# Kernel tuning notes

Measured on AMD Instinct MI355X. Metric: run time of the kernel, lower is better.

Reference implementation:

```python
import jax, jax.numpy as jnp
import numpy as np

NUM_HEADS = 8
EPS = 1e-12  # torch F.normalize default eps


def setup_inputs() -> dict:
    key = jax.random.key(0)
    k0, k1, k2, k3 = jax.random.split(key, 4)
    b, c, d, h, w = 2, 64, 8, 128, 128
    x = jax.random.normal(k0, (b, c, d, h, w), dtype=jnp.float32)
    # 1x1x1 conv weights stored as [out, in]; depthwise 3x3x3 as [out, 1, kd, kh, kw]
    w_qkv = jax.random.normal(k1, (3 * c, c), dtype=jnp.float32) * 0.05
    w_dw = jax.random.normal(k2, (3 * c, 1, 3, 3, 3), dtype=jnp.float32) * 0.05
    temperature = jnp.ones((NUM_HEADS, 1, 1), dtype=jnp.float32)
    w_proj = jax.random.normal(k3, (c, c), dtype=jnp.float32) * 0.05
    return {"x": x, "w_qkv": w_qkv, "w_dw": w_dw, "temperature": temperature, "w_proj": w_proj}


def _l2norm(t):
    # F.normalize(t, dim=-1): t / max(||t||, eps)
    n = jnp.sqrt(jnp.sum(t * t, axis=-1, keepdims=True))
    return t / jnp.maximum(n, EPS)


def reference(x, w_qkv, w_dw, temperature, w_proj):
    b, c, d, h, w = x.shape
    heads = NUM_HEADS
    ch = c // heads  # per-head channel dim
    # 1x1x1 conv (pointwise) -> einsum over channels
    qkv = jnp.einsum('bcdhw,oc->bodhw', x, w_qkv)
    # depthwise 3x3x3 conv, padding 1 (SAME), groups = 3*c
    qkv = jax.lax.conv_general_dilated(
        qkv, w_dw, window_strides=(1, 1, 1), padding=[(1, 1)] * 3,
        feature_group_count=3 * c,
        dimension_numbers=('NCDHW', 'OIDHW', 'NCDHW'))
    q, k, v = jnp.split(qkv, 3, axis=1)
    n = d * h * w
    q = q.reshape(b, heads, ch, n)
    k = k.reshape(b, heads, ch, n)
    v = v.reshape(b, heads, ch, n)
    q = _l2norm(q)
    k = _l2norm(k)
    # channel-channel attention: [b, heads, ch, ch]
    attn = jnp.einsum('bhcn,bhen->bhce', q, k) * temperature
    attn = jax.nn.softmax(attn, axis=-1)
    out = jnp.einsum('bhce,bhen->bhcn', attn, v)
    out = out.reshape(b, c, d, h, w)
    out = jnp.einsum('bcdhw,oc->bodhw', out, w_proj)
    return out
```

## Files before the change

kernel.cpp:

```cpp
#include <hip/hip_runtime.h>
#include <math.h>

#define NPOS 131072
#define GC 128

typedef __attribute__((ext_vector_type(8))) short short8v;
typedef __attribute__((ext_vector_type(4))) float f32x4;
typedef __attribute__((address_space(3))) unsigned int lds_u32;
typedef const __attribute__((address_space(1))) unsigned int glb_u32;

__device__ __forceinline__ void bf16split(float x, unsigned short& hi, unsigned short& lo) {
  unsigned u = __float_as_uint(x);
  hi = (unsigned short)(u >> 16);
  float hif = __uint_as_float(u & 0xffff0000u);
  float l = x - hif;
  lo = (unsigned short)(__float_as_uint(l) >> 16);
}

__global__ void k_prep(const float* __restrict__ w_qkv, unsigned short* __restrict__ whi,
                       unsigned short* __restrict__ wlo) {
  int idx = blockIdx.x * 256 + threadIdx.x;
  if (idx < 12288) {
    int j = idx & 7, l = (idx >> 3) & 63, ks = (idx >> 9) & 1, ot = (idx >> 10) & 3,
        g = idx >> 12;
    int out = ot * 16 + (l & 15);
    int k = ks * 32 + (l >> 4) * 8 + j;
    bf16split(w_qkv[(g * 64 + out) * 64 + k], whi[idx], wlo[idx]);
  }
}

__device__ __forceinline__ void stage_async(const float* __restrict__ gb, float* lbuf,
                                            int tid) {
#pragma unroll
  for (int r = 0; r < 4; ++r) {
    int idx = r * 256 + tid;
    int ch = idx >> 4, f4 = idx & 15;
    __builtin_amdgcn_global_load_lds((glb_u32*)(gb + (size_t)ch * NPOS + f4 * 4),
                                     (lds_u32*)(lbuf + idx * 4), 16, 0, 0);
  }
}

__device__ __forceinline__ void pw_compute(const float (*xl)[64], const short8v* ahi,
                                           const short8v* alo, float* __restrict__ ob0,
                                           int lane) {
  const int prow = lane & 15, kgrp = lane >> 4;
#pragma unroll
  for (int pt = 0; pt < 4; ++pt) {
    const int pos = pt * 16 + prow;
    short8v bh[2], bl[2];
#pragma unroll
    for (int ks = 0; ks < 2; ++ks)
#pragma unroll
      for (int j = 0; j < 8; ++j) {
        unsigned short h, lo16;
        bf16split(xl[ks * 32 + kgrp * 8 + j][pos], h, lo16);
        bh[ks][j] = (short)h;
        bl[ks][j] = (short)lo16;
      }
    f32x4 D = {0.f, 0.f, 0.f, 0.f};
#pragma unroll
    for (int ks = 0; ks < 2; ++ks) {
      D = __builtin_amdgcn_mfma_f32_16x16x32_bf16(ahi[ks], bh[ks], D, 0, 0, 0);
      D = __builtin_amdgcn_mfma_f32_16x16x32_bf16(ahi[ks], bl[ks], D, 0, 0, 0);
      D = __builtin_amdgcn_mfma_f32_16x16x32_bf16(alo[ks], bh[ks], D, 0, 0, 0);
    }
    float* ob = ob0 + pos;
#pragma unroll
    for (int jj = 0; jj < 4; ++jj) ob[(size_t)jj * NPOS] = D[jj];
  }
}

__global__ __launch_bounds__(256) void k_pw_mfma(const float* __restrict__ x,
                                                 const unsigned short* __restrict__ whi,
                                                 const unsigned short* __restrict__ wlo,
                                                 float* __restrict__ pre) {
  const int b = blockIdx.y;
  const int lane = threadIdx.x & 63;
  const int ot = threadIdx.x >> 6;
  const int p0 = blockIdx.x * 256;
  __shared__ __align__(16) float xl[2][64][64];
  short8v ahi[2], alo[2];
#pragma unroll
  for (int ks = 0; ks < 2; ++ks) {
    int fi = ((ot * 2 + ks) * 64 + lane) * 8;
    ahi[ks] = *(const short8v*)&whi[fi];
    alo[ks] = *(const short8v*)&wlo[fi];
  }
  const float* xb = x + ((size_t)b * 64) * NPOS + p0;
  const int tid = threadIdx.x;
  float* ob0 = pre + ((size_t)b * 64 + ot * 16 + (lane >> 4) * 4) * NPOS + p0;
  stage_async(xb, &xl[0][0][0], tid);
  __syncthreads();
#pragma unroll
  for (int t = 0; t < 4; ++t) {
    if (t < 3) stage_async(xb + (t + 1) * 64, &xl[(t + 1) & 1][0][0], tid);
    pw_compute(xl[t & 1], ahi, alo, ob0 + t * 64, lane);
    __syncthreads();
  }
}

__device__ __forceinline__ void stage_tile(float (*t)[10][40], const float* __restrict__ in,
                                           int h0, int w0, int tid) {
  for (int i = tid; i < 800; i += 256) {
    int j = i & 7, row = i >> 3;
    int h = row % 10, dpl = row / 10;
    int dd = dpl - 1, hh = h0 + h - 1;
    float4 v = make_float4(0.f, 0.f, 0.f, 0.f);
    if (dd >= 0 && dd < 8 && hh >= 0 && hh < 128)
      v = *(const float4*)&in[((size_t)dd * 128 + hh) * 128 + (w0 + j * 4)];
    *(float4*)&t[dpl][h][4 + j * 4] = v;
  }
  for (int i = tid; i < 200; i += 256) {
    int side = i & 1, row = i >> 1;
    int h = row % 10, dpl = row / 10;
    int dd = dpl - 1, hh = h0 + h - 1;
    int ww = side ? (w0 + 32) : (w0 - 1);
    float v = 0.f;
    if (dd >= 0 && dd < 8 && hh >= 0 && hh < 128 && ww >= 0 && ww < 128)
      v = in[((size_t)dd * 128 + hh) * 128 + ww];
    t[dpl][h][side ? 36 : 3] = v;
  }
}

__device__ __forceinline__ void conv_droll(const float (*t)[10][40], const float* wk,
                                           int hl, int wl, float* acc) {
#pragma unroll
  for (int d = 0; d < 8; ++d) acc[d] = 0.f;
#pragma unroll
  for (int dpl = 0; dpl < 10; ++dpl) {
#pragma unroll
    for (int kh = 0; kh < 3; ++kh) {
#pragma unroll
      for (int kw = 0; kw < 3; ++kw) {
        float f = t[dpl][hl + kh][3 + wl + kw];
#pragma unroll
        for (int kd = 0; kd < 3; ++kd) {
          const int d = dpl - kd;
          if (d >= 0 && d < 8)
            acc[d] = fmaf(f, wk[(kd * 3 + kh) * 3 + kw], acc[d]);
        }
      }
    }
  }
}

__global__ __launch_bounds__(256) void k_dw(const float* __restrict__ pre,
                                            const float* __restrict__ w_dw,
                                            float* __restrict__ conv,
                                            float* __restrict__ nsq, int g) {
  const int id = blockIdx.x;
  const int sid = (id & 7) * 1024 + (id >> 3);
  const int z = sid >> 6, r = sid & 63, by = r >> 2, bx = r & 3;
  const int b = z >> 6;
  const int c = z & 63;
  const int h0 = by * 8;
  const int w0 = bx * 32;
  __shared__ float t[10][10][40];
  __shared__ float red[4];
  const int tid = threadIdx.y * 32 + threadIdx.x;
  stage_tile(t, pre + ((size_t)b * 64 + c) * NPOS, h0, w0, tid);
  float wk[27];
#pragma unroll
  for (int i = 0; i < 27; ++i) wk[i] = w_dw[(g * 64 + c) * 27 + i];
  __syncthreads();
  const int wl = threadIdx.x, hl = threadIdx.y;
  float acc[8];
  conv_droll(t, wk, hl, wl, acc);
  float* outp = conv + ((size_t)b * 64 + c) * NPOS + (size_t)(h0 + hl) * 128 + (w0 + wl);
  float nsum = 0.f;
#pragma unroll
  for (int d = 0; d < 8; ++d) {
    outp[(size_t)d * 16384] = acc[d];
    nsum = fmaf(acc[d], acc[d], nsum);
  }
  if (nsq) {
    const int lane = tid & 63, wv = tid >> 6;
    float v = nsum;
    v += __shfl_down(v, 32); v += __shfl_down(v, 16); v += __shfl_down(v, 8);
    v += __shfl_down(v, 4);  v += __shfl_down(v, 2);  v += __shfl_down(v, 1);
    if (lane == 0) red[wv] = v;
    __syncthreads();
    if (tid == 0) {
      const int blk = by * 4 + bx;
      nsq[((size_t)b * 64 + c) * 64 + blk] = red[0] + red[1] + red[2] + red[3];
    }
  }
}

__global__ __launch_bounds__(256) void k_gramS(const float* __restrict__ qconv,
                                               const float* __restrict__ kconv,
                                               float* __restrict__ partialS) {
  const int chunk = blockIdx.x;
  const int bh = blockIdx.y;
  const int b = bh >> 3, head = bh & 7;
  const int tid = threadIdx.x;
  const size_t base = ((size_t)b * 64 + head * 8) * NPOS + (size_t)chunk * 1024 + tid;
  const float* qb = qconv + base;
  const float* kb = kconv + base;
  float S[64];
#pragma unroll
  for (int i = 0; i < 64; ++i) S[i] = 0.f;
#pragma unroll
  for (int it = 0; it < 4; ++it) {
    const size_t off = (size_t)it * 256;
    float qv[8], kv[8];
#pragma unroll
    for (int c = 0; c < 8; ++c) qv[c] = qb[(size_t)c * NPOS + off];
#pragma unroll
    for (int e = 0; e < 8; ++e) kv[e] = kb[(size_t)e * NPOS + off];
#pragma unroll
    for (int c = 0; c < 8; ++c)
#pragma unroll
      for (int e = 0; e < 8; ++e) S[c * 8 + e] = fmaf(qv[c], kv[e], S[c * 8 + e]);
  }
#pragma unroll
  for (int i = 0; i < 64; ++i) asm volatile("" : "+v"(S[i]));

  const int lane = tid & 63, wv = tid >> 6;
#define BSTEP(src, dst, n, s)                                        \
  {                                                                  \
    const bool hi_ = (lane >> (s)) & 1;                              \
    _Pragma("unroll")                                                \
    for (int i_ = 0; i_ < (n); ++i_) {                               \
      float send_ = hi_ ? src[i_] : src[i_ + (n)];                   \
      float mine_ = hi_ ? src[i_ + (n)] : src[i_];                   \
      dst[i_] = mine_ + __shfl_xor(send_, 1 << (s));                 \
    }                                                                \
  }
  float v32[32], v16[16], v8[8], v4[4], v2[2], v1[1];
  BSTEP(S,   v32, 32, 0)
  BSTEP(v32, v16, 16, 1)
  BSTEP(v16, v8,   8, 2)
  BSTEP(v8,  v4,   4, 3)
  BSTEP(v4,  v2,   2, 4)
  BSTEP(v2,  v1,   1, 5)
#undef BSTEP
  const int idx = ((lane & 1) << 5) | ((lane & 2) << 3) | ((lane & 4) << 1) |
                  ((lane & 8) >> 1) | ((lane & 16) >> 3) | ((lane & 32) >> 5);
  __shared__ float red[4][64];
  red[wv][idx] = v1[0];
  __syncthreads();
  if (tid < 64) {
    float s = red[0][tid] + red[1][tid] + red[2][tid] + red[3][tid];
    partialS[((size_t)bh * GC + chunk) * 64 + tid] = s;
  }
}

__global__ void k_attn(const float* __restrict__ partialS, const float* __restrict__ nqp,
                       const float* __restrict__ nkp, const float* __restrict__ temp,
                       float* __restrict__ A) {
  const int bh = blockIdx.x;
  const int b = bh >> 3, head = bh & 7;
  const int tid = threadIdx.x;
  __shared__ float sums[80];
  if (tid < 64) {
    float s = 0.f;
    const float* pp = partialS + (size_t)bh * GC * 64 + tid;
    for (int j = 0; j < GC; ++j) s += pp[j * 64];
    sums[tid] = s;
  } else if (tid < 72) {
    const int e = tid - 64;
    float s = 0.f;
    const float* pp = nkp + ((size_t)b * 64 + head * 8 + e) * 64;
    for (int j = 0; j < 64; ++j) s += pp[j];
    sums[64 + e] = s;
  } else if (tid < 80) {
    const int c = tid - 72;
    float s = 0.f;
    const float* pp = nqp + ((size_t)b * 64 + head * 8 + c) * 64;
    for (int j = 0; j < 64; ++j) s += pp[j];
    sums[72 + c] = s;
  }
  __syncthreads();
  if (tid < 8) {
    const int c = tid;
    float tp = temp[head];
    float qd = fmaxf(sqrtf(sums[72 + c]), 1e-12f);
    float vals[8];
    float mx = -1e30f;
#pragma unroll
    for (int e = 0; e < 8; ++e) {
      float kd = fmaxf(sqrtf(sums[64 + e]), 1e-12f);
      vals[e] = sums[c * 8 + e] / (qd * kd) * tp;
      mx = fmaxf(mx, vals[e]);
    }
    float den = 0.f;
#pragma unroll
    for (int e = 0; e < 8; ++e) { vals[e] = expf(vals[e] - mx); den += vals[e]; }
#pragma unroll
    for (int e = 0; e < 8; ++e) A[bh * 64 + c * 8 + e] = vals[e] / den;
  }
}

__global__ void k_M(const float* __restrict__ w_proj, const float* __restrict__ A,
                    unsigned short* __restrict__ Mhi, unsigned short* __restrict__ Mlo) {
  const int b = blockIdx.x;
  for (int e = threadIdx.x; e < 4096; e += 256) {
    int j = e & 7, l = (e >> 3) & 63, ks = (e >> 9) & 1, ot = (e >> 10) & 3;
    int out = ot * 16 + (l & 15);
    int gch = ks * 32 + (l >> 4) * 8 + j;
    int hg = gch >> 3, jj = gch & 7;
    float s = 0.f;
#pragma unroll
    for (int i = 0; i < 8; ++i)
      s += w_proj[out * 64 + hg * 8 + i] * A[(b * 8 + hg) * 64 + i * 8 + jj];
    bf16split(s, Mhi[b * 4096 + e], Mlo[b * 4096 + e]);
  }
}

__global__ __launch_bounds__(256) void k_out_mfma(const float* __restrict__ vconv,
                                                  const unsigned short* __restrict__ Mhi,
                                                  const unsigned short* __restrict__ Mlo,
                                                  float* __restrict__ out) {
  const int b = blockIdx.y;
  const int lane = threadIdx.x & 63;
  const int ot = threadIdx.x >> 6;
  const int p0 = blockIdx.x * 256;
  __shared__ __align__(16) float xl[2][64][64];
  short8v ahi[2], alo[2];
#pragma unroll
  for (int ks = 0; ks < 2; ++ks) {
    int fi = b * 4096 + ((ot * 2 + ks) * 64 + lane) * 8;
    ahi[ks] = *(const short8v*)&Mhi[fi];
    alo[ks] = *(const short8v*)&Mlo[fi];
  }
  const float* vb = vconv + ((size_t)b * 64) * NPOS + p0;
  const int tid = threadIdx.x;
  float* ob0 = out + ((size_t)b * 64 + ot * 16 + (lane >> 4) * 4) * NPOS + p0;
  stage_async(vb, &xl[0][0][0], tid);
  __syncthreads();
#pragma unroll
  for (int t = 0; t < 4; ++t) {
    if (t < 3) stage_async(vb + (t + 1) * 64, &xl[(t + 1) & 1][0][0], tid);
    pw_compute(xl[t & 1], ahi, alo, ob0 + t * 64, lane);
    __syncthreads();
  }
}

extern "C" void kernel_launch(void* const* d_in, const int* in_sizes, int n_in,
                              void* d_out, int out_size, void* d_ws, size_t ws_size,
                              hipStream_t stream) {
  const float* x      = (const float*)d_in[0];
  const float* w_qkv  = (const float*)d_in[1];
  const float* w_dw   = (const float*)d_in[2];
  const float* temp   = (const float*)d_in[3];
  const float* w_proj = (const float*)d_in[4];
  float* out = (float*)d_out;
  float* ws  = (float*)d_ws;

  float* conv_buf = ws;
  float* kconv    = conv_buf + 16777216ull;
  float* nqp      = kconv + 16777216ull;
  float* nkp      = nqp + 8192ull;
  float* partialS = nkp + 8192ull;
  float* Abuf     = partialS + 131072ull;
  unsigned short* whi = (unsigned short*)(Abuf + 1024ull);
  unsigned short* wlo = whi + 12288ull;
  unsigned short* Mhi = wlo + 12288ull;
  unsigned short* Mlo = Mhi + 8192ull;

  k_prep<<<48, 256, 0, stream>>>(w_qkv, whi, wlo);
  k_pw_mfma<<<dim3(512, 2), 256, 0, stream>>>(x, whi, wlo, out);
  k_dw<<<8192, dim3(32, 8), 0, stream>>>(out, w_dw, conv_buf, nqp, 0);
  k_pw_mfma<<<dim3(512, 2), 256, 0, stream>>>(x, whi + 4096, wlo + 4096, out);
  k_dw<<<8192, dim3(32, 8), 0, stream>>>(out, w_dw, kconv, nkp, 1);
  k_gramS<<<dim3(GC, 16), 256, 0, stream>>>(conv_buf, kconv, partialS);
  k_attn<<<16, 128, 0, stream>>>(partialS, nqp, nkp, temp, Abuf);
  k_M<<<2, 256, 0, stream>>>(w_proj, Abuf, Mhi, Mlo);
  k_pw_mfma<<<dim3(512, 2), 256, 0, stream>>>(x, whi + 8192, wlo + 8192, out);
  k_dw<<<8192, dim3(32, 8), 0, stream>>>(out, w_dw, conv_buf, nullptr, 2);
  k_out_mfma<<<dim3(512, 2), 256, 0, stream>>>(conv_buf, Mhi, Mlo, out);
}
```

Baseline: 231.9 us.

## Stage pointwise MFMA outputs through LDS for coalesced stores, one tile per block

```diff
diff --git a/kernel.cpp b/kernel.cpp
--- a/kernel.cpp
+++ b/kernel.cpp
@@ -6,8 +6,6 @@
 
 typedef __attribute__((ext_vector_type(8))) short short8v;
 typedef __attribute__((ext_vector_type(4))) float f32x4;
-typedef __attribute__((address_space(3))) unsigned int lds_u32;
-typedef const __attribute__((address_space(1))) unsigned int glb_u32;
 
 __device__ __forceinline__ void bf16split(float x, unsigned short& hi, unsigned short& lo) {
   unsigned u = __float_as_uint(x);
@@ -29,21 +27,22 @@
   }
 }
 
-__device__ __forceinline__ void stage_async(const float* __restrict__ gb, float* lbuf,
-                                            int tid) {
+__device__ __forceinline__ void pw_body(const float* __restrict__ gin,
+                                        const short8v* ahi, const short8v* alo,
+                                        float* __restrict__ gout, int tid) {
+  __shared__ __align__(16) float xl[64][66];
+  const int lane = tid & 63;
+  const int ot = tid >> 6;
+  const int f4 = tid & 15;
 #pragma unroll
   for (int r = 0; r < 4; ++r) {
-    int idx = r * 256 + tid;
-    int ch = idx >> 4, f4 = idx & 15;
-    __builtin_amdgcn_global_load_lds((glb_u32*)(gb + (size_t)ch * NPOS + f4 * 4),
-                                     (lds_u32*)(lbuf + idx * 4), 16, 0, 0);
-  }
-}
-
-__device__ __forceinline__ void pw_compute(const float (*xl)[64], const short8v* ahi,
-                                           const short8v* alo, float* __restrict__ ob0,
-                                           int lane) {
+    int ch2 = (r * 256 + tid) >> 4;
+    float4 g = *(const float4*)&gin[(size_t)ch2 * NPOS + f4 * 4];
+    *(float4*)&xl[ch2][f4 * 4] = g;
+  }
+  __syncthreads();
   const int prow = lane & 15, kgrp = lane >> 4;
+  f32x4 Dv[4];
 #pragma unroll
   for (int pt = 0; pt < 4; ++pt) {
     const int pos = pt * 16 + prow;
@@ -64,9 +63,20 @@
       D = __builtin_amdgcn_mfma_f32_16x16x32_bf16(ahi[ks], bl[ks], D, 0, 0, 0);
       D = __builtin_amdgcn_mfma_f32_16x16x32_bf16(alo[ks], bh[ks], D, 0, 0, 0);
     }
-    float* ob = ob0 + pos;
-#pragma unroll
-    for (int jj = 0; jj < 4; ++jj) ob[(size_t)jj * NPOS] = D[jj];
+    Dv[pt] = D;
+  }
+  __syncthreads();
+#pragma unroll
+  for (int pt = 0; pt < 4; ++pt)
+#pragma unroll
+    for (int jj = 0; jj < 4; ++jj)
+      xl[ot * 16 + kgrp * 4 + jj][pt * 16 + prow] = Dv[pt][jj];
+  __syncthreads();
+#pragma unroll
+  for (int r = 0; r < 4; ++r) {
+    int idx = r * 256 + tid;
+    int row = idx >> 4;
+    *(float4*)&gout[(size_t)row * NPOS + f4 * 4] = *(const float4*)&xl[row][f4 * 4];
   }
 }
 
@@ -77,8 +87,7 @@
   const int b = blockIdx.y;
   const int lane = threadIdx.x & 63;
   const int ot = threadIdx.x >> 6;
-  const int p0 = blockIdx.x * 256;
-  __shared__ __align__(16) float xl[2][64][64];
+  const int p0 = blockIdx.x * 64;
   short8v ahi[2], alo[2];
 #pragma unroll
   for (int ks = 0; ks < 2; ++ks) {
@@ -86,17 +95,8 @@
     ahi[ks] = *(const short8v*)&whi[fi];
     alo[ks] = *(const short8v*)&wlo[fi];
   }
-  const float* xb = x + ((size_t)b * 64) * NPOS + p0;
-  const int tid = threadIdx.x;
-  float* ob0 = pre + ((size_t)b * 64 + ot * 16 + (lane >> 4) * 4) * NPOS + p0;
-  stage_async(xb, &xl[0][0][0], tid);
-  __syncthreads();
-#pragma unroll
-  for (int t = 0; t < 4; ++t) {
-    if (t < 3) stage_async(xb + (t + 1) * 64, &xl[(t + 1) & 1][0][0], tid);
-    pw_compute(xl[t & 1], ahi, alo, ob0 + t * 64, lane);
-    __syncthreads();
-  }
+  pw_body(x + ((size_t)b * 64) * NPOS + p0, ahi, alo,
+          pre + ((size_t)b * 64) * NPOS + p0, threadIdx.x);
 }
 
 __device__ __forceinline__ void stage_tile(float (*t)[10][40], const float* __restrict__ in,
@@ -315,8 +315,7 @@
   const int b = blockIdx.y;
   const int lane = threadIdx.x & 63;
   const int ot = threadIdx.x >> 6;
-  const int p0 = blockIdx.x * 256;
-  __shared__ __align__(16) float xl[2][64][64];
+  const int p0 = blockIdx.x * 64;
   short8v ahi[2], alo[2];
 #pragma unroll
   for (int ks = 0; ks < 2; ++ks) {
@@ -324,17 +323,8 @@
     ahi[ks] = *(const short8v*)&Mhi[fi];
     alo[ks] = *(const short8v*)&Mlo[fi];
   }
-  const float* vb = vconv + ((size_t)b * 64) * NPOS + p0;
-  const int tid = threadIdx.x;
-  float* ob0 = out + ((size_t)b * 64 + ot * 16 + (lane >> 4) * 4) * NPOS + p0;
-  stage_async(vb, &xl[0][0][0], tid);
-  __syncthreads();
-#pragma unroll
-  for (int t = 0; t < 4; ++t) {
-    if (t < 3) stage_async(vb + (t + 1) * 64, &xl[(t + 1) & 1][0][0], tid);
-    pw_compute(xl[t & 1], ahi, alo, ob0 + t * 64, lane);
-    __syncthreads();
-  }
+  pw_body(vconv + ((size_t)b * 64) * NPOS + p0, ahi, alo,
+          out + ((size_t)b * 64) * NPOS + p0, threadIdx.x);
 }
 
 extern "C" void kernel_launch(void* const* d_in, const int* in_sizes, int n_in,
@@ -360,14 +350,14 @@
   unsigned short* Mlo = Mhi + 8192ull;
 
   k_prep<<<48, 256, 0, stream>>>(w_qkv, whi, wlo);
-  k_pw_mfma<<<dim3(512, 2), 256, 0, stream>>>(x, whi, wlo, out);
+  k_pw_mfma<<<dim3(2048, 2), 256, 0, stream>>>(x, whi, wlo, out);
   k_dw<<<8192, dim3(32, 8), 0, stream>>>(out, w_dw, conv_buf, nqp, 0);
-  k_pw_mfma<<<dim3(512, 2), 256, 0, stream>>>(x, whi + 4096, wlo + 4096, out);
+  k_pw_mfma<<<dim3(2048, 2), 256, 0, stream>>>(x, whi + 4096, wlo + 4096, out);
   k_dw<<<8192, dim3(32, 8), 0, stream>>>(out, w_dw, kconv, nkp, 1);
   k_gramS<<<dim3(GC, 16), 256, 0, stream>>>(conv_buf, kconv, partialS);
   k_attn<<<16, 128, 0, stream>>>(partialS, nqp, nkp, temp, Abuf);
   k_M<<<2, 256, 0, stream>>>(w_proj, Abuf, Mhi, Mlo);
-  k_pw_mfma<<<dim3(512, 2), 256, 0, stream>>>(x, whi + 8192, wlo + 8192, out);
+  k_pw_mfma<<<dim3(2048, 2), 256, 0, stream>>>(x, whi + 8192, wlo + 8192, out);
   k_dw<<<8192, dim3(32, 8), 0, stream>>>(out, w_dw, conv_buf, nullptr, 2);
-  k_out_mfma<<<dim3(512, 2), 256, 0, stream>>>(conv_buf, Mhi, Mlo, out);
-}
+  k_out_mfma<<<dim3(2048, 2), 256, 0, stream>>>(conv_buf, Mhi, Mlo, out);
+}
```

After: 222.8 us. -3.9%, faster.
